# Optimization experiments

Measured on AMD Instinct MI355X. Metric: run time of the kernel, lower is better.

## Reference

```python
import jax, jax.numpy as jnp
import numpy as np

B = 4096      # batch
IN = 512      # input_size
HS = [256, 128, 64]  # hidden_sizes (num liquid neurons per layer)
S = 64        # liquid_state_size
OUT = 12      # output_size


def setup_inputs() -> dict:
    key = jax.random.key(0)
    keys = iter(jax.random.split(key, 40))

    def rn(shape, scale=0.05):
        return jax.random.normal(next(keys), shape, dtype=jnp.float32) * scale

    inp = {"x": jax.random.normal(next(keys), (B, IN), dtype=jnp.float32)}
    sizes = [IN] + HS
    for l, (din, n) in enumerate(zip(sizes[:-1], sizes[1:])):
        inp[f"Wi{l}"] = rn((n, din, S))   # stacked input_projection weights
        inp[f"bi{l}"] = rn((n, S))        # input_projection biases
        inp[f"bl{l}"] = rn((n, S))        # liquid_state biases (hidden starts at 0)
        inp[f"Wo{l}"] = rn((n, S))        # output_projection weights (out dim 1)
        inp[f"bo{l}"] = rn((n,))          # output_projection biases
        inp[f"L{l}"]  = rn((n, n), 0.1)   # lateral_weights
        inp[f"a{l}"]  = jnp.ones((n,), jnp.float32)  # adaptation_state
    inp["Wout"] = rn((HS[-1], OUT))
    inp["bout"] = rn((OUT,))
    return inp


def _liquid_layer(x, Wi, bi, bl, Wo, bo, L, a):
    # Stacked over neurons n: liquid_input[b,n,s] = x @ Wi_n + bi_n + bl_n
    li = jnp.einsum('bi,nis->bns', x, Wi) + bi[None] + bl[None]
    act = jnp.tanh(li) + 0.1 * jnp.sin(0.5 * li) * jnp.cos(0.3 * li)
    # per-neuron scalar output projection -> [B, N]
    out = jnp.einsum('bns,ns->bn', act, Wo) + bo
    # lateral mixing + adaptation scaling
    out = out + 0.1 * (out @ L)
    return out * a


def reference(x, Wi0, bi0, bl0, Wo0, bo0, L0, a0,
              Wi1, bi1, bl1, Wo1, bo1, L1, a1,
              Wi2, bi2, bl2, Wo2, bo2, L2, a2,
              Wout, bout):
    h = _liquid_layer(x, Wi0, bi0, bl0, Wo0, bo0, L0, a0)
    h = _liquid_layer(h, Wi1, bi1, bl1, Wo1, bo1, L1, a1)
    h = _liquid_layer(h, Wi2, bi2, bl2, Wo2, bo2, L2, a2)
    return h @ Wout + bout
```

## Files before the change

kernel.cpp:

```cpp
#include <hip/hip_runtime.h>
#include <hip/hip_bf16.h>
#include <math.h>


#define BATCH 4096

typedef __bf16 bf16x8 __attribute__((ext_vector_type(8)));
typedef float floatx4 __attribute__((ext_vector_type(4)));

__device__ __forceinline__ void gl_lds16(const void* g, void* l) {
    __builtin_amdgcn_global_load_lds(
        (const __attribute__((address_space(1))) void*)g,
        (__attribute__((address_space(3))) void*)l, 16, 0, 0);
}

__device__ __forceinline__ float act_exact(float v) {
    return tanhf(v) + 0.1f * sinf(0.5f * v) * cosf(0.3f * v);
}


__device__ __forceinline__ void wconv_tile(const float* __restrict__ Wi,
                                           __hip_bfloat16* __restrict__ Wt,
                                           const float* __restrict__ a,
                                           int K, int n, int k0, int t)
{
    __shared__ float lds[64][65];
    const float* src = Wi + ((size_t)n * K + k0) * 64;
#pragma unroll
    for (int i = 0; i < 4; ++i) {
        int idx = t + i * 256;
        int r = idx >> 4;
        int s4 = (idx & 15) * 4;
        float4 v = *(const float4*)(src + (size_t)r * 64 + s4);
        if (a) {
            float av = a[k0 + r];
            v.x *= av; v.y *= av; v.z *= av; v.w *= av;
        }
        lds[s4 + 0][r] = v.x;
        lds[s4 + 1][r] = v.y;
        lds[s4 + 2][r] = v.z;
        lds[s4 + 3][r] = v.w;
    }
    __syncthreads();
    __hip_bfloat16* dst = Wt + (size_t)n * 64 * K + k0;
#pragma unroll
    for (int i = 0; i < 4; ++i) {
        int idx = t + i * 256;
        int s = idx >> 4;
        int k4 = (idx & 15) * 4;
        union { ushort4 u4; __hip_bfloat16 b[4]; } o;
        o.b[0] = __float2bfloat16(lds[s][k4 + 0]);
        o.b[1] = __float2bfloat16(lds[s][k4 + 1]);
        o.b[2] = __float2bfloat16(lds[s][k4 + 2]);
        o.b[3] = __float2bfloat16(lds[s][k4 + 3]);
        *(ushort4*)(dst + (size_t)s * K + k4) = o.u4;
    }
}

__global__ __launch_bounds__(256) void conv_all(
    const float* __restrict__ x, __hip_bfloat16* __restrict__ xb,
    const float* __restrict__ Wi0, const float* __restrict__ Wi1,
    const float* __restrict__ Wi2,
    const float* __restrict__ a0, const float* __restrict__ a1,
    const float* __restrict__ L0, const float* __restrict__ L1,
    const float* __restrict__ L2, const float* __restrict__ a2,
    const float* __restrict__ Wout,
    __hip_bfloat16* __restrict__ Wt0, __hip_bfloat16* __restrict__ G1,
    __hip_bfloat16* __restrict__ G2,
    __hip_bfloat16* __restrict__ Lb0, __hip_bfloat16* __restrict__ Lb1,
    float* __restrict__ Tg, float* __restrict__ Wfin)
{
    int bid = blockIdx.x;
    int t = threadIdx.x;
    if (bid < 2048) {
        int g = bid * 256 + t;
        float4 v = ((const float4*)x)[g];
        union { ushort4 u4; __hip_bfloat16 b[4]; } o;
        o.b[0] = __float2bfloat16(v.x);
        o.b[1] = __float2bfloat16(v.y);
        o.b[2] = __float2bfloat16(v.z);
        o.b[3] = __float2bfloat16(v.w);
        ((ushort4*)xb)[g] = o.u4;
    } else if (bid < 4096) {
        int r = bid - 2048;
        wconv_tile(Wi0, Wt0, nullptr, 512, r >> 3, (r & 7) * 64, t);
    } else if (bid < 4608) {
        int r = bid - 4096;
        wconv_tile(Wi1, G1, a0, 256, r >> 2, (r & 3) * 64, t);
    } else if (bid < 4736) {
        int r = bid - 4608;
        wconv_tile(Wi2, G2, a1, 128, r >> 1, (r & 1) * 64, t);
    } else if (bid == 4736) {
#pragma unroll
        for (int i = 0; i < 2; ++i) {
            int e = t + 256 * i;
            float v0 = (float)(e - 256) * 0.03125f;
            Tg[2 * e] = act_exact(v0);
            Tg[2 * e + 1] = act_exact(v0 + 0.03125f);
        }
    } else if (bid < 4801) {
        int g = (bid - 4737) * 1024 + t * 4;
        float4 v = *(const float4*)(L0 + g);
        union { ushort4 u4; __hip_bfloat16 b[4]; } o;
        o.b[0] = __float2bfloat16(v.x);
        o.b[1] = __float2bfloat16(v.y);
        o.b[2] = __float2bfloat16(v.z);
        o.b[3] = __float2bfloat16(v.w);
        *(ushort4*)(Lb0 + g) = o.u4;
    } else if (bid < 4817) {
        int g = (bid - 4801) * 1024 + t * 4;
        float4 v = *(const float4*)(L1 + g);
        union { ushort4 u4; __hip_bfloat16 b[4]; } o;
        o.b[0] = __float2bfloat16(v.x);
        o.b[1] = __float2bfloat16(v.y);
        o.b[2] = __float2bfloat16(v.z);
        o.b[3] = __float2bfloat16(v.w);
        *(ushort4*)(Lb1 + g) = o.u4;
    } else {
#pragma unroll
        for (int i = 0; i < 3; ++i) {
            int e = t + 256 * i;
            int mm = e / 12, o = e - 12 * mm;
            float acc = a2[mm] * Wout[mm * 12 + o];
            float s = 0.f;
            for (int nn = 0; nn < 64; ++nn)
                s += L2[mm * 64 + nn] * a2[nn] * Wout[nn * 12 + o];
            Wfin[e] = acc + 0.1f * s;
        }
    }
}


__global__ __launch_bounds__(512, 4) void liquid_proj_mfma(
    const __hip_bfloat16* __restrict__ X,
    const __hip_bfloat16* __restrict__ Wt,
    const float* __restrict__ bi, const float* __restrict__ bl,
    const float* __restrict__ Wo, const float* __restrict__ bo,
    const float* __restrict__ Tg,
    __hip_bfloat16* __restrict__ t, int K, int Nn)
{
    __shared__ __align__(16) __hip_bfloat16 As[128 * 64];
    __shared__ __align__(16) __hip_bfloat16 Bs[256 * 64];
    __shared__ __align__(16) float Tt[1024];

    const int tid = threadIdx.x;
    const int wid = tid >> 6;
    const int wb = wid & 1;
    const int wn = wid >> 1;
    const int lane = tid & 63;
    const int m = lane & 15;
    const int qd = lane >> 4;

    const int bid = blockIdx.x;
    const int xcd = bid & 7;
    const int sw = bid >> 3;
    const int n_grp = sw >> 2;
    const int row_grp = ((sw & 3) << 3) | xcd;
    const int row0 = row_grp * 128;
    const int n0 = n_grp * 4;
    const int n = n0 + wn;

    if (tid < 256)
        gl_lds16(Tg + tid * 4, (void*)(Tt + tid * 4));

    floatx4 acc[4][4];
#pragma unroll
    for (int rt = 0; rt < 4; ++rt) {
        int sb = n * 64 + rt * 16 + qd * 4;
        float4 b4i = *(const float4*)(bi + sb);
        float4 b4l = *(const float4*)(bl + sb);
        floatx4 b4 = {b4i.x + b4l.x, b4i.y + b4l.y, b4i.z + b4l.z, b4i.w + b4l.w};
#pragma unroll
        for (int ct = 0; ct < 4; ++ct)
            acc[rt][ct] = b4;
    }

    const int ar0 = tid >> 3;
    const int aq0 = (tid & 7) ^ (ar0 & 7);
    const int ar1 = (tid + 512) >> 3;
    const int aq1 = ((tid + 512) & 7) ^ (ar1 & 7);
    const __hip_bfloat16* Xr0 = X + (size_t)(row0 + ar0) * K + aq0 * 8;
    const __hip_bfloat16* Xr1 = X + (size_t)(row0 + ar1) * K + aq1 * 8;

    const __hip_bfloat16* bsrc[4];
#pragma unroll
    for (int i = 0; i < 4; ++i) {
        int Li = i * 512 + tid;
        int c = Li >> 3;
        int q = (Li & 7) ^ (c & 7);
        bsrc[i] = Wt + ((size_t)(n0 + (c >> 6)) * 64 + (c & 63)) * K + q * 8;
    }

    for (int k0 = 0; k0 < K; k0 += 64) {
        gl_lds16(Xr0 + k0, (void*)(As + tid * 8));
        gl_lds16(Xr1 + k0, (void*)(As + ((size_t)tid + 512) * 8));
#pragma unroll
        for (int i = 0; i < 4; ++i)
            gl_lds16(bsrc[i] + k0, (void*)(Bs + ((size_t)i * 512 + tid) * 8));
        __syncthreads();
#pragma unroll
        for (int kk = 0; kk < 2; ++kk) {
            bf16x8 af[4], bfr[4];
#pragma unroll
            for (int rt = 0; rt < 4; ++rt) {
                int sr = wn * 64 + rt * 16 + m;
                int slot = sr * 8 + ((kk * 4 + qd) ^ (sr & 7));
                af[rt] = *(const bf16x8*)(Bs + slot * 8);
            }
#pragma unroll
            for (int ct = 0; ct < 4; ++ct) {
                int br = wb * 64 + ct * 16 + m;
                int slot = br * 8 + ((kk * 4 + qd) ^ (br & 7));
                bfr[ct] = *(const bf16x8*)(As + slot * 8);
            }
#pragma unroll
            for (int rt = 0; rt < 4; ++rt)
#pragma unroll
                for (int ct = 0; ct < 4; ++ct)
                    acc[rt][ct] = __builtin_amdgcn_mfma_f32_16x16x32_bf16(
                        af[rt], bfr[ct], acc[rt][ct], 0, 0, 0);
        }
        __syncthreads();
    }

    float wo[4][4];
#pragma unroll
    for (int rt = 0; rt < 4; ++rt) {
        float4 w4 = *(const float4*)(Wo + n * 64 + rt * 16 + qd * 4);
        wo[rt][0] = w4.x; wo[rt][1] = w4.y; wo[rt][2] = w4.z; wo[rt][3] = w4.w;
    }
    float bov = bo[n];
    float p[4] = {0.f, 0.f, 0.f, 0.f};
    const float2* Tt2 = (const float2*)Tt;
#pragma unroll
    for (int ct = 0; ct < 4; ++ct)
#pragma unroll
        for (int rt = 0; rt < 4; ++rt)
#pragma unroll
            for (int reg = 0; reg < 4; ++reg) {
                float v = acc[rt][ct][reg];
                float u = fmaf(v, 32.f, 256.f);
                u = fminf(fmaxf(u, 0.f), 510.99f);
                float fi = floorf(u);
                int ii = (int)fi;
                float fr = u - fi;
                float2 pr = Tt2[ii];
                p[ct] = fmaf(fmaf(fr, pr.y - pr.x, pr.x), wo[rt][reg], p[ct]);
            }
#pragma unroll
    for (int ct = 0; ct < 4; ++ct) {
        p[ct] += __shfl_xor(p[ct], 16, 64);
        p[ct] += __shfl_xor(p[ct], 32, 64);
    }
    if (qd == 0) {
#pragma unroll
        for (int ct = 0; ct < 4; ++ct)
            t[(size_t)(row0 + wb * 64 + ct * 16 + m) * Nn + n] =
                __float2bfloat16(p[ct] + bov);
    }
}


__global__ __launch_bounds__(512, 4) void fold_lateral(
    const __hip_bfloat16* __restrict__ G1, const __hip_bfloat16* __restrict__ Lb0,
    __hip_bfloat16* __restrict__ W1,
    const __hip_bfloat16* __restrict__ G2, const __hip_bfloat16* __restrict__ Lb1,
    __hip_bfloat16* __restrict__ W2)
{
    __shared__ __align__(16) __hip_bfloat16 As[128 * 64];
    __shared__ __align__(16) __hip_bfloat16 Bs[256 * 64];

    const int bid = blockIdx.x;
    const __hip_bfloat16* G;
    const __hip_bfloat16* Lb;
    __hip_bfloat16* W;
    int r0, e0, K;
    if (bid < 64) {
        G = G1; Lb = Lb0; W = W1; K = 256;
        r0 = (bid >> 1) * 256; e0 = (bid & 1) * 128;
    } else {
        G = G2; Lb = Lb1; W = W2; K = 128;
        r0 = (bid - 64) * 256; e0 = 0;
    }

    const int tid = threadIdx.x;
    const int wid = tid >> 6;
    const int wb = wid & 1;
    const int wn = wid >> 1;
    const int lane = tid & 63;
    const int m = lane & 15;
    const int qd = lane >> 4;

    floatx4 acc[4][4];
#pragma unroll
    for (int rt = 0; rt < 4; ++rt)
#pragma unroll
        for (int ct = 0; ct < 4; ++ct)
            acc[rt][ct] = {0.f, 0.f, 0.f, 0.f};

    const int ar0 = tid >> 3;
    const int aq0 = (tid & 7) ^ (ar0 & 7);
    const int ar1 = (tid + 512) >> 3;
    const int aq1 = ((tid + 512) & 7) ^ (ar1 & 7);
    const __hip_bfloat16* Xr0 = Lb + (size_t)(e0 + ar0) * K + aq0 * 8;
    const __hip_bfloat16* Xr1 = Lb + (size_t)(e0 + ar1) * K + aq1 * 8;

    const __hip_bfloat16* bsrc[4];
#pragma unroll
    for (int i = 0; i < 4; ++i) {
        int Li = i * 512 + tid;
        int c = Li >> 3;
        int q = (Li & 7) ^ (c & 7);
        bsrc[i] = G + (size_t)(r0 + c) * K + q * 8;
    }

    for (int k0 = 0; k0 < K; k0 += 64) {
        gl_lds16(Xr0 + k0, (void*)(As + tid * 8));
        gl_lds16(Xr1 + k0, (void*)(As + ((size_t)tid + 512) * 8));
#pragma unroll
        for (int i = 0; i < 4; ++i)
            gl_lds16(bsrc[i] + k0, (void*)(Bs + ((size_t)i * 512 + tid) * 8));
        __syncthreads();
#pragma unroll
        for (int kk = 0; kk < 2; ++kk) {
            bf16x8 af[4], bfr[4];
#pragma unroll
            for (int rt = 0; rt < 4; ++rt) {
                int sr = wn * 64 + rt * 16 + m;
                int slot = sr * 8 + ((kk * 4 + qd) ^ (sr & 7));
                af[rt] = *(const bf16x8*)(Bs + slot * 8);
            }
#pragma unroll
            for (int ct = 0; ct < 4; ++ct) {
                int br = wb * 64 + ct * 16 + m;
                int slot = br * 8 + ((kk * 4 + qd) ^ (br & 7));
                bfr[ct] = *(const bf16x8*)(As + slot * 8);
            }
#pragma unroll
            for (int rt = 0; rt < 4; ++rt)
#pragma unroll
                for (int ct = 0; ct < 4; ++ct)
                    acc[rt][ct] = __builtin_amdgcn_mfma_f32_16x16x32_bf16(
                        af[rt], bfr[ct], acc[rt][ct], 0, 0, 0);
        }
        __syncthreads();
    }

#pragma unroll
    for (int rt = 0; rt < 4; ++rt)
#pragma unroll
        for (int ct = 0; ct < 4; ++ct)
#pragma unroll
            for (int reg = 0; reg < 4; ++reg) {
                int rl = wn * 64 + rt * 16 + qd * 4 + reg;
                int el = wb * 64 + ct * 16 + m;
                size_t gi = (size_t)(r0 + rl) * K + (e0 + el);
                W[gi] = __float2bfloat16(
                    __bfloat162float(G[gi]) + 0.1f * acc[rt][ct][reg]);
            }
}


__global__ __launch_bounds__(256) void out_head(
    const __hip_bfloat16* __restrict__ t2,
    const float* __restrict__ Wfin,
    const float* __restrict__ bout,
    float* __restrict__ y)
{
    __shared__ float hb[16][65];
    __shared__ float wf[768];
    __shared__ float bo[12];

    const int tid = threadIdx.x;
    const int row0 = blockIdx.x * 16;

#pragma unroll
    for (int i = 0; i < 4; ++i) {
        int idx = tid + i * 256;
        int r = idx >> 6;
        int c = idx & 63;
        hb[r][c] = __bfloat162float(t2[(size_t)(row0 + r) * 64 + c]);
    }
#pragma unroll
    for (int i = 0; i < 3; ++i)
        wf[tid + 256 * i] = Wfin[tid + 256 * i];
    if (tid < 12) bo[tid] = bout[tid];
    __syncthreads();

    if (tid < 192) {
        int r = tid / 12, o = tid - 12 * r;
        float acc = bo[o];
#pragma unroll
        for (int k = 0; k < 64; ++k)
            acc += hb[r][k] * wf[k * 12 + o];
        y[(size_t)(row0 + r) * 12 + o] = acc;
    }
}


__global__ __launch_bounds__(256) void liquid_proj_f32(
    const float* __restrict__ x, const float* __restrict__ Wi,
    const float* __restrict__ bi, const float* __restrict__ bl,
    const float* __restrict__ Wo, const float* __restrict__ bo,
    float* __restrict__ t, int K, int Nn)
{
    __shared__ float xs[16][65];
    __shared__ float ws[16][65];
    const int tid = threadIdx.x;
    const int tx = tid & 15, ty = tid >> 4;
    const int row0 = blockIdx.x * 64;
    const int n = blockIdx.y;
    const float* Wn = Wi + (size_t)n * K * 64;
    float acc[4][4] = {};
    for (int k0 = 0; k0 < K; k0 += 16) {
#pragma unroll
        for (int i = 0; i < 4; ++i) {
            int li = tid + 256 * i;
            xs[li & 15][li >> 4] = x[(size_t)(row0 + (li >> 4)) * K + k0 + (li & 15)];
        }
#pragma unroll
        for (int i = 0; i < 4; ++i) {
            int li = tid + 256 * i;
            ws[li >> 6][li & 63] = Wn[(size_t)(k0 + (li >> 6)) * 64 + (li & 63)];
        }
        __syncthreads();
#pragma unroll
        for (int kk = 0; kk < 16; ++kk) {
            float xa[4], wb[4];
#pragma unroll
            for (int i = 0; i < 4; ++i) xa[i] = xs[kk][4 * ty + i];
#pragma unroll
            for (int j = 0; j < 4; ++j) wb[j] = ws[kk][4 * tx + j];
#pragma unroll
            for (int i = 0; i < 4; ++i)
#pragma unroll
                for (int j = 0; j < 4; ++j) acc[i][j] += xa[i] * wb[j];
        }
        __syncthreads();
    }
    float part[4] = {0.f, 0.f, 0.f, 0.f};
#pragma unroll
    for (int j = 0; j < 4; ++j) {
        int cc = 4 * tx + j;
        float bias = bi[n * 64 + cc] + bl[n * 64 + cc];
        float wov = Wo[n * 64 + cc];
#pragma unroll
        for (int i = 0; i < 4; ++i) {
            float v = acc[i][j] + bias;
            part[i] += (tanhf(v) + 0.1f * sinf(0.5f * v) * cosf(0.3f * v)) * wov;
        }
    }
#pragma unroll
    for (int mk = 1; mk < 16; mk <<= 1)
#pragma unroll
        for (int i = 0; i < 4; ++i) part[i] += __shfl_xor(part[i], mk, 64);
    if (tx == 0) {
        float b = bo[n];
#pragma unroll
        for (int i = 0; i < 4; ++i)
            t[(size_t)(row0 + 4 * ty + i) * Nn + n] = part[i] + b;
    }
}

__global__ void lateral_f32_kernel(const float* __restrict__ t,
                                   const float* __restrict__ L,
                                   const float* __restrict__ a,
                                   float* __restrict__ h, int Nn)
{
    extern __shared__ float tb[];
    const int b = blockIdx.x;
    const int n = threadIdx.x;
    tb[n] = t[(size_t)b * Nn + n];
    __syncthreads();
    float acc = 0.f;
    for (int mm = 0; mm < Nn; ++mm)
        acc += tb[mm] * L[(size_t)mm * Nn + n];
    h[(size_t)b * Nn + n] = (tb[n] + 0.1f * acc) * a[n];
}

__global__ void out_f32_kernel(const float* __restrict__ h,
                               const float* __restrict__ Wout,
                               const float* __restrict__ bout,
                               float* __restrict__ y)
{
    int g = blockIdx.x * blockDim.x + threadIdx.x;
    if (g >= BATCH * 12) return;
    int b = g / 12, o = g - 12 * b;
    float acc = bout[o];
    const float* hb = h + (size_t)b * 64;
#pragma unroll
    for (int k = 0; k < 64; ++k) acc += hb[k] * Wout[k * 12 + o];
    y[g] = acc;
}

extern "C" void kernel_launch(void* const* d_in, const int* in_sizes, int n_in,
                              void* d_out, int out_size, void* d_ws, size_t ws_size,
                              hipStream_t stream)
{
    (void)in_sizes; (void)n_in; (void)out_size;
    const float* x = (const float*)d_in[0];
    const float* Wout = (const float*)d_in[22];
    const float* bout = (const float*)d_in[23];
    const int dims[4] = {512, 256, 128, 64};
    char* ws = (char*)d_ws;
    const size_t MB = 1024u * 1024u;
    const size_t KB = 1024u;

    if (ws_size >= 28 * MB) {
        __hip_bfloat16* Wt0 = (__hip_bfloat16*)ws;
        __hip_bfloat16* G1  = (__hip_bfloat16*)(ws + 16 * MB);
        __hip_bfloat16* G2  = (__hip_bfloat16*)(ws + 20 * MB);
        __hip_bfloat16* xb  = (__hip_bfloat16*)(ws + 21 * MB);
        __hip_bfloat16* W1f = (__hip_bfloat16*)(ws + 21 * MB);
        __hip_bfloat16* t0  = (__hip_bfloat16*)(ws + 25 * MB);
        __hip_bfloat16* t1  = (__hip_bfloat16*)ws;
        __hip_bfloat16* W2f = (__hip_bfloat16*)(ws + 2 * MB);
        __hip_bfloat16* t2  = (__hip_bfloat16*)(ws + 4 * MB);
        float* Tg = (float*)(ws + 27 * MB);
        __hip_bfloat16* Lb0 = (__hip_bfloat16*)(ws + 27 * MB + 16 * KB);
        __hip_bfloat16* Lb1 = (__hip_bfloat16*)(ws + 27 * MB + 160 * KB);
        float* Wfin = (float*)(ws + 27 * MB + 256 * KB);

        const float* a0 = (const float*)d_in[7];
        const float* a1 = (const float*)d_in[14];
        const float* L0 = (const float*)d_in[6];
        const float* L1 = (const float*)d_in[13];
        const float* L2 = (const float*)d_in[20];
        const float* a2 = (const float*)d_in[21];

        conv_all<<<4818, 256, 0, stream>>>(
            x, xb, (const float*)d_in[1], (const float*)d_in[8],
            (const float*)d_in[15], a0, a1, L0, L1, L2, a2, Wout,
            Wt0, G1, G2, Lb0, Lb1, Tg, Wfin);

        liquid_proj_mfma<<<2048, 512, 0, stream>>>(
            xb, Wt0, (const float*)d_in[2], (const float*)d_in[3],
            (const float*)d_in[4], (const float*)d_in[5], Tg, t0, 512, 256);

        fold_lateral<<<80, 512, 0, stream>>>(G1, Lb0, W1f, G2, Lb1, W2f);

        liquid_proj_mfma<<<1024, 512, 0, stream>>>(
            t0, W1f, (const float*)d_in[9], (const float*)d_in[10],
            (const float*)d_in[11], (const float*)d_in[12], Tg, t1, 256, 128);

        liquid_proj_mfma<<<512, 512, 0, stream>>>(
            t1, W2f, (const float*)d_in[16], (const float*)d_in[17],
            (const float*)d_in[18], (const float*)d_in[19], Tg, t2, 128, 64);

        out_head<<<BATCH / 16, 256, 0, stream>>>(t2, Wfin, bout, (float*)d_out);
    } else {
        float* tbufs[3] = {(float*)ws, (float*)ws, (float*)(ws + 4 * MB)};
        float* hs[3] = {(float*)(ws + 4 * MB), (float*)(ws + 2 * MB),
                        (float*)(ws + 5 * MB)};
        const float* prev = x;
        for (int l = 0; l < 3; ++l) {
            const float* Wi = (const float*)d_in[1 + 7 * l + 0];
            const float* bi = (const float*)d_in[1 + 7 * l + 1];
            const float* bl = (const float*)d_in[1 + 7 * l + 2];
            const float* Wo = (const float*)d_in[1 + 7 * l + 3];
            const float* bo = (const float*)d_in[1 + 7 * l + 4];
            const float* L  = (const float*)d_in[1 + 7 * l + 5];
            const float* a  = (const float*)d_in[1 + 7 * l + 6];
            const int K = dims[l], Nn = dims[l + 1];
            liquid_proj_f32<<<dim3(BATCH / 64, Nn), 256, 0, stream>>>(
                prev, Wi, bi, bl, Wo, bo, tbufs[l], K, Nn);
            lateral_f32_kernel<<<BATCH, Nn, Nn * sizeof(float), stream>>>(
                tbufs[l], L, a, hs[l], Nn);
            prev = hs[l];
        }
        out_f32_kernel<<<(BATCH * 12 + 255) / 256, 256, 0, stream>>>(
            hs[2], Wout, bout, (float*)d_out);
    }
}
```

Measured before the change: 252.0 us.

## Fuse lateral folding into layer-0 projection and output head into layer-2 projection

Moves the lateral-weight folding GEMMs into extra blocks of the layer-0 projection launch and updates G1/G2 in place, dropping the separate fold kernel and its output buffers. The output head is fused into the last projection kernel: a per-row-group atomic counter lets the last finishing block compute the final 12-wide outputs. This removes two kernel launches and their serialization gaps. In exchange it adds atomics, fences, counter resets in conv_all, and lower declared occupancy (launch bounds 2) for the fused kernels.

```diff
diff --git a/kernel.cpp b/kernel.cpp
--- a/kernel.cpp
+++ b/kernel.cpp
@@ -68,7 +68,7 @@
     __hip_bfloat16* __restrict__ Wt0, __hip_bfloat16* __restrict__ G1,
     __hip_bfloat16* __restrict__ G2,
     __hip_bfloat16* __restrict__ Lb0, __hip_bfloat16* __restrict__ Lb1,
-    float* __restrict__ Tg, float* __restrict__ Wfin)
+    float* __restrict__ Tg, float* __restrict__ Wfin, int* __restrict__ cnt)
 {
     int bid = blockIdx.x;
     int t = threadIdx.x;
@@ -117,6 +117,7 @@
         o.b[3] = __float2bfloat16(v.w);
         *(ushort4*)(Lb1 + g) = o.u4;
     } else {
+        if (t < 32) cnt[t] = 0;
 #pragma unroll
         for (int i = 0; i < 3; ++i) {
             int e = t + 256 * i;
@@ -131,18 +132,14 @@
 }
 
 
-__global__ __launch_bounds__(512, 4) void liquid_proj_mfma(
-    const __hip_bfloat16* __restrict__ X,
+__device__ __forceinline__ void proj_tile(
+    int bid, const __hip_bfloat16* __restrict__ X,
     const __hip_bfloat16* __restrict__ Wt,
     const float* __restrict__ bi, const float* __restrict__ bl,
     const float* __restrict__ Wo, const float* __restrict__ bo,
-    const float* __restrict__ Tg,
-    __hip_bfloat16* __restrict__ t, int K, int Nn)
-{
-    __shared__ __align__(16) __hip_bfloat16 As[128 * 64];
-    __shared__ __align__(16) __hip_bfloat16 Bs[256 * 64];
-    __shared__ __align__(16) float Tt[1024];
-
+    __hip_bfloat16* __restrict__ t, int K, int Nn,
+    __hip_bfloat16* As, __hip_bfloat16* Bs, const float* Tt)
+{
     const int tid = threadIdx.x;
     const int wid = tid >> 6;
     const int wb = wid & 1;
@@ -151,7 +148,6 @@
     const int m = lane & 15;
     const int qd = lane >> 4;
 
-    const int bid = blockIdx.x;
     const int xcd = bid & 7;
     const int sw = bid >> 3;
     const int n_grp = sw >> 2;
@@ -159,9 +155,6 @@
     const int row0 = row_grp * 128;
     const int n0 = n_grp * 4;
     const int n = n0 + wn;
-
-    if (tid < 256)
-        gl_lds16(Tg + tid * 4, (void*)(Tt + tid * 4));
 
     floatx4 acc[4][4];
 #pragma unroll
@@ -261,28 +254,98 @@
 }
 
 
-__global__ __launch_bounds__(512, 4) void fold_lateral(
-    const __hip_bfloat16* __restrict__ G1, const __hip_bfloat16* __restrict__ Lb0,
-    __hip_bfloat16* __restrict__ W1,
-    const __hip_bfloat16* __restrict__ G2, const __hip_bfloat16* __restrict__ Lb1,
-    __hip_bfloat16* __restrict__ W2)
-{
-    __shared__ __align__(16) __hip_bfloat16 As[128 * 64];
-    __shared__ __align__(16) __hip_bfloat16 Bs[256 * 64];
-
-    const int bid = blockIdx.x;
-    const __hip_bfloat16* G;
-    const __hip_bfloat16* Lb;
-    __hip_bfloat16* W;
-    int r0, e0, K;
-    if (bid < 64) {
-        G = G1; Lb = Lb0; W = W1; K = 256;
-        r0 = (bid >> 1) * 256; e0 = (bid & 1) * 128;
-    } else {
-        G = G2; Lb = Lb1; W = W2; K = 128;
-        r0 = (bid - 64) * 256; e0 = 0;
-    }
-
+__device__ __forceinline__ void fold1_tile(
+    int fb, __hip_bfloat16* __restrict__ G,
+    const __hip_bfloat16* __restrict__ Lb,
+    __hip_bfloat16* As, __hip_bfloat16* Bs)
+{
+    const int K = 256;
+    const int r0 = fb * 128;
+    const int tid = threadIdx.x;
+    const int wid = tid >> 6;
+    const int we = wid & 3;
+    const int wn = wid >> 2;
+    const int lane = tid & 63;
+    const int m = lane & 15;
+    const int qd = lane >> 4;
+
+    floatx4 acc[4][4];
+#pragma unroll
+    for (int rt = 0; rt < 4; ++rt)
+#pragma unroll
+        for (int ct = 0; ct < 4; ++ct)
+            acc[rt][ct] = {0.f, 0.f, 0.f, 0.f};
+
+    const int ar0 = tid >> 3;
+    const int aq0 = (tid & 7) ^ (ar0 & 7);
+    const int ar1 = (tid + 512) >> 3;
+    const int aq1 = ((tid + 512) & 7) ^ (ar1 & 7);
+    const __hip_bfloat16* Xr0 = G + (size_t)(r0 + ar0) * K + aq0 * 8;
+    const __hip_bfloat16* Xr1 = G + (size_t)(r0 + ar1) * K + aq1 * 8;
+
+    const __hip_bfloat16* bsrc[4];
+#pragma unroll
+    for (int i = 0; i < 4; ++i) {
+        int Li = i * 512 + tid;
+        int c = Li >> 3;
+        int q = (Li & 7) ^ (c & 7);
+        bsrc[i] = Lb + (size_t)c * K + q * 8;
+    }
+
+    for (int k0 = 0; k0 < K; k0 += 64) {
+        gl_lds16(Xr0 + k0, (void*)(As + tid * 8));
+        gl_lds16(Xr1 + k0, (void*)(As + ((size_t)tid + 512) * 8));
+#pragma unroll
+        for (int i = 0; i < 4; ++i)
+            gl_lds16(bsrc[i] + k0, (void*)(Bs + ((size_t)i * 512 + tid) * 8));
+        __syncthreads();
+#pragma unroll
+        for (int kk = 0; kk < 2; ++kk) {
+            bf16x8 af[4], bfr[4];
+#pragma unroll
+            for (int rt = 0; rt < 4; ++rt) {
+                int sr = wn * 64 + rt * 16 + m;
+                int slot = sr * 8 + ((kk * 4 + qd) ^ (sr & 7));
+                af[rt] = *(const bf16x8*)(As + slot * 8);
+            }
+#pragma unroll
+            for (int ct = 0; ct < 4; ++ct) {
+                int br = we * 64 + ct * 16 + m;
+                int slot = br * 8 + ((kk * 4 + qd) ^ (br & 7));
+                bfr[ct] = *(const bf16x8*)(Bs + slot * 8);
+            }
+#pragma unroll
+            for (int rt = 0; rt < 4; ++rt)
+#pragma unroll
+                for (int ct = 0; ct < 4; ++ct)
+                    acc[rt][ct] = __builtin_amdgcn_mfma_f32_16x16x32_bf16(
+                        af[rt], bfr[ct], acc[rt][ct], 0, 0, 0);
+        }
+        __syncthreads();
+    }
+
+#pragma unroll
+    for (int rt = 0; rt < 4; ++rt)
+#pragma unroll
+        for (int ct = 0; ct < 4; ++ct)
+#pragma unroll
+            for (int reg = 0; reg < 4; ++reg) {
+                int rl = wn * 64 + rt * 16 + qd * 4 + reg;
+                int el = we * 64 + ct * 16 + m;
+                size_t gi = (size_t)(r0 + rl) * K + el;
+                G[gi] = __float2bfloat16(
+                    __bfloat162float(G[gi]) + 0.1f * acc[rt][ct][reg]);
+            }
+}
+
+
+__device__ __forceinline__ void fold2_tile(
+    int fb, __hip_bfloat16* __restrict__ G,
+    const __hip_bfloat16* __restrict__ Lb,
+    __hip_bfloat16* As, __hip_bfloat16* Bs)
+{
+    const int K = 128;
+    const int r0 = fb * 256;
     const int tid = threadIdx.x;
     const int wid = tid >> 6;
     const int wb = wid & 1;
@@ -302,8 +365,8 @@
     const int aq0 = (tid & 7) ^ (ar0 & 7);
     const int ar1 = (tid + 512) >> 3;
     const int aq1 = ((tid + 512) & 7) ^ (ar1 & 7);
-    const __hip_bfloat16* Xr0 = Lb + (size_t)(e0 + ar0) * K + aq0 * 8;
-    const __hip_bfloat16* Xr1 = Lb + (size_t)(e0 + ar1) * K + aq1 * 8;
+    const __hip_bfloat16* Xr0 = Lb + (size_t)ar0 * K + aq0 * 8;
+    const __hip_bfloat16* Xr1 = Lb + (size_t)ar1 * K + aq1 * 8;
 
     const __hip_bfloat16* bsrc[4];
 #pragma unroll
@@ -354,46 +417,108 @@
             for (int reg = 0; reg < 4; ++reg) {
                 int rl = wn * 64 + rt * 16 + qd * 4 + reg;
                 int el = wb * 64 + ct * 16 + m;
-                size_t gi = (size_t)(r0 + rl) * K + (e0 + el);
-                W[gi] = __float2bfloat16(
+                size_t gi = (size_t)(r0 + rl) * K + el;
+                G[gi] = __float2bfloat16(
                     __bfloat162float(G[gi]) + 0.1f * acc[rt][ct][reg]);
             }
 }
 
 
-__global__ __launch_bounds__(256) void out_head(
-    const __hip_bfloat16* __restrict__ t2,
-    const float* __restrict__ Wfin,
-    const float* __restrict__ bout,
-    float* __restrict__ y)
-{
-    __shared__ float hb[16][65];
-    __shared__ float wf[768];
-    __shared__ float bo[12];
-
+__global__ __launch_bounds__(512, 2) void proj0_fold(
+    const __hip_bfloat16* __restrict__ X, const __hip_bfloat16* __restrict__ Wt,
+    const float* __restrict__ bi, const float* __restrict__ bl,
+    const float* __restrict__ Wo, const float* __restrict__ bo,
+    const float* __restrict__ Tg, __hip_bfloat16* __restrict__ t0,
+    __hip_bfloat16* __restrict__ G1, const __hip_bfloat16* __restrict__ Lb0,
+    __hip_bfloat16* __restrict__ G2, const __hip_bfloat16* __restrict__ Lb1)
+{
+    __shared__ __align__(16) __hip_bfloat16 As[128 * 64];
+    __shared__ __align__(16) __hip_bfloat16 Bs[256 * 64];
+    __shared__ __align__(16) float Tt[1024];
+    const int bid = blockIdx.x;
+    if (bid < 2048) {
+        if (threadIdx.x < 256)
+            gl_lds16(Tg + threadIdx.x * 4, (void*)(Tt + threadIdx.x * 4));
+        proj_tile(bid, X, Wt, bi, bl, Wo, bo, t0, 512, 256, As, Bs, Tt);
+    } else if (bid < 2112) {
+        fold1_tile(bid - 2048, G1, Lb0, As, Bs);
+    } else {
+        fold2_tile(bid - 2112, G2, Lb1, As, Bs);
+    }
+}
+
+
+__global__ __launch_bounds__(512, 4) void liquid_proj_mfma(
+    const __hip_bfloat16* __restrict__ X, const __hip_bfloat16* __restrict__ Wt,
+    const float* __restrict__ bi, const float* __restrict__ bl,
+    const float* __restrict__ Wo, const float* __restrict__ bo,
+    const float* __restrict__ Tg, __hip_bfloat16* __restrict__ t, int K, int Nn)
+{
+    __shared__ __align__(16) __hip_bfloat16 As[128 * 64];
+    __shared__ __align__(16) __hip_bfloat16 Bs[256 * 64];
+    __shared__ __align__(16) float Tt[1024];
+    if (threadIdx.x < 256)
+        gl_lds16(Tg + threadIdx.x * 4, (void*)(Tt + threadIdx.x * 4));
+    proj_tile(blockIdx.x, X, Wt, bi, bl, Wo, bo, t, K, Nn, As, Bs, Tt);
+}
+
+
+__global__ __launch_bounds__(512, 2) void proj2_head(
+    const __hip_bfloat16* __restrict__ X, const __hip_bfloat16* __restrict__ Wt,
+    const float* __restrict__ bi, const float* __restrict__ bl,
+    const float* __restrict__ Wo, const float* __restrict__ bo,
+    const float* __restrict__ Tg, __hip_bfloat16* __restrict__ t2,
+    int* __restrict__ cnt, const float* __restrict__ Wfin,
+    const float* __restrict__ bout, float* __restrict__ y)
+{
+    __shared__ __align__(16) __hip_bfloat16 As[128 * 64];
+    __shared__ __align__(16) __hip_bfloat16 Bs[256 * 64];
+    __shared__ __align__(16) float Tt[1024];
+    __shared__ int flag;
+
+    const int bid = blockIdx.x;
+    if (threadIdx.x < 256)
+        gl_lds16(Tg + threadIdx.x * 4, (void*)(Tt + threadIdx.x * 4));
+    proj_tile(bid, X, Wt, bi, bl, Wo, bo, t2, 128, 64, As, Bs, Tt);
+
+    const int xcd = bid & 7;
+    const int sw = bid >> 3;
+    const int row_grp = ((sw & 3) << 3) | xcd;
     const int tid = threadIdx.x;
-    const int row0 = blockIdx.x * 16;
-
-#pragma unroll
-    for (int i = 0; i < 4; ++i) {
-        int idx = tid + i * 256;
-        int r = idx >> 6;
-        int c = idx & 63;
-        hb[r][c] = __bfloat162float(t2[(size_t)(row0 + r) * 64 + c]);
-    }
-#pragma unroll
-    for (int i = 0; i < 3; ++i)
-        wf[tid + 256 * i] = Wfin[tid + 256 * i];
-    if (tid < 12) bo[tid] = bout[tid];
+
     __syncthreads();
-
-    if (tid < 192) {
-        int r = tid / 12, o = tid - 12 * r;
-        float acc = bo[o];
-#pragma unroll
-        for (int k = 0; k < 64; ++k)
-            acc += hb[r][k] * wf[k * 12 + o];
-        y[(size_t)(row0 + r) * 12 + o] = acc;
+    if (tid == 0) {
+        __threadfence();
+        flag = atomicAdd(&cnt[row_grp], 1);
+    }
+    __syncthreads();
+    if (flag == 15) {
+        __threadfence();
+        const int row0 = row_grp * 128;
+#pragma unroll
+        for (int i = 0; i < 2; ++i) {
+            int idx = tid + i * 512;
+            gl_lds16(t2 + ((size_t)(row0 + (idx >> 3)) * 64 + (idx & 7) * 8),
+                     (void*)(As + (size_t)idx * 8));
+        }
+#pragma unroll
+        for (int i = 0; i < 2; ++i) {
+            int j = tid + i * 512;
+            if (j < 768) Tt[j] = Wfin[j];
+        }
+        if (tid < 12) Tt[768 + tid] = bout[tid];
+        __syncthreads();
+#pragma unroll
+        for (int j = 0; j < 3; ++j) {
+            int oi = tid + j * 512;
+            int r = oi / 12, o = oi - 12 * r;
+            float acc = Tt[768 + o];
+            const __hip_bfloat16* row = As + r * 64;
+#pragma unroll
+            for (int k = 0; k < 64; ++k)
+                acc += __bfloat162float(row[k]) * Tt[k * 12 + o];
+            y[(size_t)(row0 + r) * 12 + o] = acc;
+        }
     }
 }
 
@@ -511,15 +636,14 @@
         __hip_bfloat16* G1  = (__hip_bfloat16*)(ws + 16 * MB);
         __hip_bfloat16* G2  = (__hip_bfloat16*)(ws + 20 * MB);
         __hip_bfloat16* xb  = (__hip_bfloat16*)(ws + 21 * MB);
-        __hip_bfloat16* W1f = (__hip_bfloat16*)(ws + 21 * MB);
         __hip_bfloat16* t0  = (__hip_bfloat16*)(ws + 25 * MB);
         __hip_bfloat16* t1  = (__hip_bfloat16*)ws;
-        __hip_bfloat16* W2f = (__hip_bfloat16*)(ws + 2 * MB);
         __hip_bfloat16* t2  = (__hip_bfloat16*)(ws + 4 * MB);
         float* Tg = (float*)(ws + 27 * MB);
         __hip_bfloat16* Lb0 = (__hip_bfloat16*)(ws + 27 * MB + 16 * KB);
         __hip_bfloat16* Lb1 = (__hip_bfloat16*)(ws + 27 * MB + 160 * KB);
         float* Wfin = (float*)(ws + 27 * MB + 256 * KB);
+        int* cnt = (int*)(ws + 27 * MB + 260 * KB);
 
         const float* a0 = (const float*)d_in[7];
         const float* a1 = (const float*)d_in[14];
@@ -531,23 +655,21 @@
         conv_all<<<4818, 256, 0, stream>>>(
             x, xb, (const float*)d_in[1], (const float*)d_in[8],
             (const float*)d_in[15], a0, a1, L0, L1, L2, a2, Wout,
-            Wt0, G1, G2, Lb0, Lb1, Tg, Wfin);
-
-        liquid_proj_mfma<<<2048, 512, 0, stream>>>(
+            Wt0, G1, G2, Lb0, Lb1, Tg, Wfin, cnt);
+
+        proj0_fold<<<2128, 512, 0, stream>>>(
             xb, Wt0, (const float*)d_in[2], (const float*)d_in[3],
-            (const float*)d_in[4], (const float*)d_in[5], Tg, t0, 512, 256);
-
-        fold_lateral<<<80, 512, 0, stream>>>(G1, Lb0, W1f, G2, Lb1, W2f);
+            (const float*)d_in[4], (const float*)d_in[5], Tg, t0,
+            G1, Lb0, G2, Lb1);
 
         liquid_proj_mfma<<<1024, 512, 0, stream>>>(
-            t0, W1f, (const float*)d_in[9], (const float*)d_in[10],
+            t0, G1, (const float*)d_in[9], (const float*)d_in[10],
             (const float*)d_in[11], (const float*)d_in[12], Tg, t1, 256, 128);
 
-        liquid_proj_mfma<<<512, 512, 0, stream>>>(
-            t1, W2f, (const float*)d_in[16], (const float*)d_in[17],
-            (const float*)d_in[18], (const float*)d_in[19], Tg, t2, 128, 64);
-
-        out_head<<<BATCH / 16, 256, 0, stream>>>(t2, Wfin, bout, (float*)d_out);
+        proj2_head<<<512, 512, 0, stream>>>(
+            t1, G2, (const float*)d_in[16], (const float*)d_in[17],
+            (const float*)d_in[18], (const float*)d_in[19], Tg, t2,
+            cnt, Wfin, bout, (float*)d_out);
     } else {
         float* tbufs[3] = {(float*)ws, (float*)ws, (float*)(ws + 4 * MB)};
         float* hs[3] = {(float*)(ws + 4 * MB), (float*)(ws + 2 * MB),
```

Result: slower. 308.1 us (+22.3%).
